# Performance work log

Measured on AMD Instinct MI355X. Metric: run time of the kernel, lower is better.

Reference implementation:

```python
import jax, jax.numpy as jnp
import numpy as np


def setup_inputs() -> dict:
    key = jax.random.key(0)
    ks = jax.random.split(key, 9)
    B, Q, K, F, C = 16, 2048, 2048, 128, 2
    q = jax.random.normal(ks[0], (B, Q, F), dtype=jnp.float32)
    k = jax.random.normal(ks[1], (B, K, F), dtype=jnp.float32)
    v = jax.random.normal(ks[2], (B, K, F), dtype=jnp.float32)
    coords_q = jax.random.uniform(ks[3], (B, Q, C), dtype=jnp.float32)
    coords_k = jax.random.uniform(ks[4], (B, K, C), dtype=jnp.float32)
    attn_mask = jax.random.randint(ks[5], (B, Q, K), 0, 2).astype(jnp.bool_)
    alibi_mask = jax.random.randint(ks[6], (B, Q, K), 0, 2).astype(jnp.bool_)
    bias_scale = jax.random.uniform(ks[7], (1,), dtype=jnp.float32)  # nn.Parameter(torch.rand(1))
    running_mean = jnp.ones((1,), dtype=jnp.float32)  # RunningMeanScaler buffer (eval mode)
    return {"q": q, "k": k, "v": v, "coords_q": coords_q, "coords_k": coords_k,
            "attn_mask": attn_mask, "alibi_mask": alibi_mask,
            "bias_scale": bias_scale, "running_mean": running_mean}


def reference(q, k, v, coords_q, coords_k, attn_mask, alibi_mask, bias_scale, running_mean):
    # [b,q,k] attention logits
    scale = jnp.asarray(k.shape[-1], q.dtype) ** -0.5
    weight_logits = jnp.einsum('bqf,bkf->bqk', q, k) * scale
    # pairwise coordinate distances [b,q,k]
    diff = coords_q[:, :, None, :] - coords_k[:, None, :, :]
    distances = jnp.sqrt(jnp.sum(diff * diff, axis=-1))
    scaled_distances = (distances / running_mean) * bias_scale  # broadcast scalars
    masked_distances = jnp.where(alibi_mask, jnp.zeros((), distances.dtype), scaled_distances)
    weights = jax.nn.softmax(weight_logits, axis=-1)
    masked = jnp.where(attn_mask, jnp.zeros((), weights.dtype), weights - masked_distances)
    attention = jnp.einsum('bqk,bkf->bqf', masked, v)
    return attention
```

## Files before the change

### kernel.cpp

```cpp
#include <hip/hip_runtime.h>
#include <stdint.h>

#define B_  16
#define QL  2048
#define KL  2048
#define FD  128
#define BQ  64
#define BK  32
#define NSTEP (KL/BK)

#define KSTR  136
#define VTOFF 4352
#define VTSTR 36
#define BUFS  8960
#define WS_HALF (B_*KL*FD)

typedef __attribute__((ext_vector_type(8))) short bf16x8;
typedef __attribute__((ext_vector_type(4))) float f32x4;
typedef __attribute__((ext_vector_type(4))) int   i32x4;
typedef __attribute__((ext_vector_type(4))) unsigned int u32x4;

__device__ __forceinline__ unsigned short f2b(float f) {
  union { float f; unsigned u; } x; x.f = f;
  return (unsigned short)((x.u + 0x8000u) >> 16);
}

__device__ __forceinline__ unsigned cvt_pk_bf16(float lo, float hi) {
  unsigned r;
  asm("v_cvt_pk_bf16_f32 %0, %1, %2" : "=v"(r) : "v"(lo), "v"(hi));
  return r;
}

__global__ __launch_bounds__(256) void conv_k(const float* __restrict__ kp,
                                              unsigned short* __restrict__ kb) {
  int idx = (blockIdx.x * 256 + threadIdx.x) * 4;
  float4 u = *(const float4*)(kp + idx);
  ushort4 s4; s4.x = f2b(u.x); s4.y = f2b(u.y); s4.z = f2b(u.z); s4.w = f2b(u.w);
  *(ushort4*)(kb + idx) = s4;
}

__global__ __launch_bounds__(256) void conv_vt(const float* __restrict__ vp,
                                               unsigned short* __restrict__ vt) {
  __shared__ float tl[32 * 132];
  const int t = threadIdx.x, b = blockIdx.x >> 6, kt = blockIdx.x & 63;
  const int r = t >> 3, f0 = (t & 7) * 16;
  const float* src = vp + ((long long)(b * KL + kt * 32 + r)) * FD + f0;
  #pragma unroll
  for (int i = 0; i < 4; ++i)
    *(float4*)&tl[r * 132 + f0 + 4 * i] = *(const float4*)(src + 4 * i);
  __syncthreads();
  const int f = t >> 1, half = t & 1;
  bf16x8 o0, o1;
  #pragma unroll
  for (int j = 0; j < 8; ++j)  o0[j] = (short)f2b(tl[(half * 16 + j) * 132 + f]);
  #pragma unroll
  for (int j = 0; j < 8; ++j)  o1[j] = (short)f2b(tl[(half * 16 + 8 + j) * 132 + f]);
  unsigned short* dst = vt + ((long long)((b * 64 + kt) * FD + f)) * 32 + half * 16;
  *(bf16x8*)dst = o0;
  *(bf16x8*)(dst + 8) = o1;
}

__global__ __launch_bounds__(256, 2) void alibi_attn(
    const unsigned short* __restrict__ kbp,
    const unsigned short* __restrict__ vtp,
    const float* __restrict__ qp,
    const float* __restrict__ cqp,
    const float* __restrict__ ckp,
    const int* __restrict__ amp,
    const int* __restrict__ almp,
    const float* __restrict__ bsp,
    const float* __restrict__ rmp,
    float* __restrict__ outp)
{
  __shared__ unsigned short kv[2 * BUFS];

  const int t    = threadIdx.x;
  const int w    = t >> 6;
  const int lane = t & 63;
  const int l15  = lane & 15;
  const int q4   = lane >> 4;

  const int bid  = blockIdx.x;
  const int xcd  = bid & 7, slot = bid >> 3;
  const int b    = (xcd << 1) | (slot >> 5);
  const int qbase = (slot & 31) * BQ;

  const float bscale = bsp[0] / rmp[0];
  const float sl2 = 0.08838834764831845f * 1.44269504089f;

  const int kr_st = t >> 3, kc_st = (t & 7) * 16;
  const int vf_st = t >> 1, vh_st = (t & 1) * 16;

  {
    const float* qg = qp + ((long long)(b * QL + qbase)) * FD;
    #pragma unroll
    for (int i = 0; i < 8; ++i) {
      int idx = t + 256 * i;
      float4 u = ((const float4*)qg)[idx];
      int row = idx >> 5, col = (idx & 31) * 4;
      ushort4 s4; s4.x = f2b(u.x); s4.y = f2b(u.y); s4.z = f2b(u.z); s4.w = f2b(u.w);
      *(ushort4*)&kv[row * KSTR + col] = s4;
    }
  }
  __syncthreads();
  bf16x8 qfrag[4];
  {
    const int m = w * 16 + l15;
    #pragma unroll
    for (int fs = 0; fs < 4; ++fs)
      qfrag[fs] = *(const bf16x8*)&kv[m * KSTR + fs * 32 + q4 * 8];
  }
  const int qrow = qbase + w * 16 + l15;
  float cqx, cqy;
  {
    float2 c2 = *(const float2*)(cqp + ((long long)(b * QL + qrow)) * 2);
    cqx = c2.x; cqy = c2.y;
  }
  const long long mrow = (long long)(b * QL + qrow) * KL;
  __syncthreads();

  const unsigned short* kgb = kbp + (long long)b * KL * FD;
  const unsigned short* vgb = vtp + (long long)b * KL * FD;

  i32x4 amv[2][2], alv[2][2];
  f32x4 ckf[2][2][2];
  bf16x8 kreg[2][2], vreg[2][2];
  const int klane0 = 4 * q4;
  #pragma unroll
  for (int s = 0; s < 2; ++s) {
    const int k0 = s * 16 + klane0;
    amv[0][s] = __builtin_nontemporal_load((const i32x4*)(amp + mrow + k0));
    alv[0][s] = __builtin_nontemporal_load((const i32x4*)(almp + mrow + k0));
    ckf[0][s][0] = *(const f32x4*)(ckp + ((long long)(b * KL + k0)) * 2);
    ckf[0][s][1] = *(const f32x4*)(ckp + ((long long)(b * KL + k0)) * 2 + 4);
  }
  {
    bf16x8 k0l = *(const bf16x8*)(kgb + kr_st * FD + kc_st);
    bf16x8 k1l = *(const bf16x8*)(kgb + kr_st * FD + kc_st + 8);
    bf16x8 v0l = *(const bf16x8*)(vgb + t * 16);
    bf16x8 v1l = *(const bf16x8*)(vgb + t * 16 + 8);
    *(bf16x8*)&kv[kr_st * KSTR + kc_st]     = k0l;
    *(bf16x8*)&kv[kr_st * KSTR + kc_st + 8] = k1l;
    *(bf16x8*)&kv[VTOFF + vf_st * VTSTR + vh_st]     = v0l;
    *(bf16x8*)&kv[VTOFF + vf_st * VTSTR + vh_st + 8] = v1l;
    kreg[1][0] = *(const bf16x8*)(kgb + (BK + kr_st) * FD + kc_st);
    kreg[1][1] = *(const bf16x8*)(kgb + (BK + kr_st) * FD + kc_st + 8);
    vreg[1][0] = *(const bf16x8*)(vgb + BK * FD + t * 16);
    vreg[1][1] = *(const bf16x8*)(vgb + BK * FD + t * 16 + 8);
  }
  __syncthreads();

  f32x4 O1[8], O2[8];
  #pragma unroll
  for (int n = 0; n < 8; ++n) {
    O1[n] = (f32x4){0.f, 0.f, 0.f, 0.f};
    O2[n] = (f32x4){0.f, 0.f, 0.f, 0.f};
  }
  float lsum = 0.f;

  const int srcA = l15 + ((q4 & 1) << 5);
  const int srcB = srcA + 16;
  const bool lowhalf = (q4 < 2);

  #pragma unroll 2
  for (int kt = 0; kt < NSTEP; ++kt) {
    const int cur = kt & 1, nxt = cur ^ 1;
    const unsigned short* kb = kv + cur * BUFS;
    unsigned short*       nb = kv + nxt * BUFS;

    const int ktf = (kt + 2 < NSTEP) ? (kt + 2) : (NSTEP - 1);
    kreg[cur][0] = *(const bf16x8*)(kgb + (ktf * BK + kr_st) * FD + kc_st);
    kreg[cur][1] = *(const bf16x8*)(kgb + (ktf * BK + kr_st) * FD + kc_st + 8);
    vreg[cur][0] = *(const bf16x8*)(vgb + ktf * (BK * FD) + t * 16);
    vreg[cur][1] = *(const bf16x8*)(vgb + ktf * (BK * FD) + t * 16 + 8);

    const int ktm = (kt + 1 < NSTEP) ? (kt + 1) : kt;
    #pragma unroll
    for (int s = 0; s < 2; ++s) {
      const int kg = ktm * BK + s * 16 + klane0;
      amv[nxt][s] = __builtin_nontemporal_load((const i32x4*)(amp + mrow + kg));
      alv[nxt][s] = __builtin_nontemporal_load((const i32x4*)(almp + mrow + kg));
      ckf[nxt][s][0] = *(const f32x4*)(ckp + ((long long)(b * KL + kg)) * 2);
      ckf[nxt][s][1] = *(const f32x4*)(ckp + ((long long)(b * KL + kg)) * 2 + 4);
    }

    f32x4 S0 = (f32x4){0.f, 0.f, 0.f, 0.f};
    f32x4 S1 = (f32x4){0.f, 0.f, 0.f, 0.f};
    #pragma unroll
    for (int fs = 0; fs < 4; ++fs) {
      bf16x8 kb0 = *(const bf16x8*)&kb[(l15)      * KSTR + fs * 32 + q4 * 8];
      bf16x8 kb1 = *(const bf16x8*)&kb[(16 + l15) * KSTR + fs * 32 + q4 * 8];
      S0 = __builtin_amdgcn_mfma_f32_16x16x32_bf16(kb0, qfrag[fs], S0, 0, 0, 0);
      S1 = __builtin_amdgcn_mfma_f32_16x16x32_bf16(kb1, qfrag[fs], S1, 0, 0, 0);
    }

    float wvv[2][4], tvv[2][4];
    #pragma unroll
    for (int s = 0; s < 2; ++s) {
      const f32x4 Sv = s ? S1 : S0;
      #pragma unroll
      for (int r = 0; r < 4; ++r) {
        float e = __builtin_amdgcn_exp2f(Sv[r] * sl2);
        lsum += e;
        const float ckx = ckf[cur][s][r >> 1][(r & 1) * 2];
        const float cky = ckf[cur][s][r >> 1][(r & 1) * 2 + 1];
        float dx = cqx - ckx, dy = cqy - cky;
        float d  = sqrtf(fmaf(dx, dx, dy * dy)) * bscale;
        int am = amv[cur][s][r], al = alv[cur][s][r];
        wvv[s][r] = am ? 0.f : e;
        tvv[s][r] = (am | al) ? 0.f : d;
      }
    }

    unsigned aX0 = cvt_pk_bf16(wvv[0][0], wvv[0][1]);
    unsigned aX1 = cvt_pk_bf16(wvv[0][2], wvv[0][3]);
    unsigned aX2 = cvt_pk_bf16(wvv[1][0], wvv[1][1]);
    unsigned aX3 = cvt_pk_bf16(wvv[1][2], wvv[1][3]);
    unsigned tX0 = cvt_pk_bf16(tvv[0][0], tvv[0][1]);
    unsigned tX1 = cvt_pk_bf16(tvv[0][2], tvv[0][3]);
    unsigned tX2 = cvt_pk_bf16(tvv[1][0], tvv[1][1]);
    unsigned tX3 = cvt_pk_bf16(tvv[1][2], tvv[1][3]);

    u32x4 wa, ta;
    {
      int y0, y2;
      y0 = __shfl((int)aX0, srcA); y2 = __shfl((int)aX2, srcA);
      wa[0] = (unsigned)(lowhalf ? y0 : y2);
      y0 = __shfl((int)aX1, srcA); y2 = __shfl((int)aX3, srcA);
      wa[1] = (unsigned)(lowhalf ? y0 : y2);
      y0 = __shfl((int)aX0, srcB); y2 = __shfl((int)aX2, srcB);
      wa[2] = (unsigned)(lowhalf ? y0 : y2);
      y0 = __shfl((int)aX1, srcB); y2 = __shfl((int)aX3, srcB);
      wa[3] = (unsigned)(lowhalf ? y0 : y2);
      y0 = __shfl((int)tX0, srcA); y2 = __shfl((int)tX2, srcA);
      ta[0] = (unsigned)(lowhalf ? y0 : y2);
      y0 = __shfl((int)tX1, srcA); y2 = __shfl((int)tX3, srcA);
      ta[1] = (unsigned)(lowhalf ? y0 : y2);
      y0 = __shfl((int)tX0, srcB); y2 = __shfl((int)tX2, srcB);
      ta[2] = (unsigned)(lowhalf ? y0 : y2);
      y0 = __shfl((int)tX1, srcB); y2 = __shfl((int)tX3, srcB);
      ta[3] = (unsigned)(lowhalf ? y0 : y2);
    }
    bf16x8 aw = __builtin_bit_cast(bf16x8, wa);
    bf16x8 at = __builtin_bit_cast(bf16x8, ta);

    #pragma unroll
    for (int n = 0; n < 8; ++n) {
      bf16x8 vb = *(const bf16x8*)&kb[VTOFF + (n * 16 + l15) * VTSTR + q4 * 8];
      O1[n] = __builtin_amdgcn_mfma_f32_16x16x32_bf16(aw, vb, O1[n], 0, 0, 0);
      O2[n] = __builtin_amdgcn_mfma_f32_16x16x32_bf16(at, vb, O2[n], 0, 0, 0);
    }

    *(bf16x8*)&nb[kr_st * KSTR + kc_st]     = kreg[nxt][0];
    *(bf16x8*)&nb[kr_st * KSTR + kc_st + 8] = kreg[nxt][1];
    *(bf16x8*)&nb[VTOFF + vf_st * VTSTR + vh_st]     = vreg[nxt][0];
    *(bf16x8*)&nb[VTOFF + vf_st * VTSTR + vh_st + 8] = vreg[nxt][1];

    asm volatile("s_waitcnt lgkmcnt(0)\n\ts_barrier" ::: "memory");
  }

  lsum += __shfl_xor(lsum, 16, 64);
  lsum += __shfl_xor(lsum, 32, 64);
  float linv[4];
  #pragma unroll
  for (int r = 0; r < 4; ++r) linv[r] = 1.0f / __shfl(lsum, q4 * 4 + r, 64);

  #pragma unroll
  for (int n = 0; n < 8; ++n) {
    #pragma unroll
    for (int r = 0; r < 4; ++r) {
      const int qg_ = qbase + w * 16 + q4 * 4 + r;
      const int f   = n * 16 + l15;
      float val = O1[n][r] * linv[r] - O2[n][r];
      __builtin_nontemporal_store(val, outp + ((long long)(b * QL + qg_)) * FD + f);
    }
  }
}

extern "C" void kernel_launch(void* const* d_in, const int* in_sizes, int n_in,
                              void* d_out, int out_size, void* d_ws, size_t ws_size,
                              hipStream_t stream) {
  const float* q   = (const float*)d_in[0];
  const float* k   = (const float*)d_in[1];
  const float* v   = (const float*)d_in[2];
  const float* cq  = (const float*)d_in[3];
  const float* ck  = (const float*)d_in[4];
  const int*   am  = (const int*)d_in[5];
  const int*   alm = (const int*)d_in[6];
  const float* bs  = (const float*)d_in[7];
  const float* rm  = (const float*)d_in[8];
  float*       out = (float*)d_out;

  unsigned short* kb = (unsigned short*)d_ws;
  unsigned short* vt = kb + WS_HALF;

  hipLaunchKernelGGL(conv_k,  dim3(WS_HALF / 1024), dim3(256), 0, stream, k, kb);
  hipLaunchKernelGGL(conv_vt, dim3(B_ * 64),        dim3(256), 0, stream, v, vt);

  dim3 grid(B_ * (QL / BQ));
  dim3 block(256);
  hipLaunchKernelGGL(alibi_attn, grid, block, 0, stream,
                     kb, vt, q, cq, ck, am, alm, bs, rm, out);
}
```

Before: 676.0 us.

## Split key dimension across two blocks and combine partial sums in extra kernel

Splits the key loop into two halves handled by separate blocks (split-K), doubling the grid from 512 to 1024 blocks. Each block writes its unnormalized partial O1/O2 and row sums to workspace, and a new combine kernel sums them and normalizes. Launch bounds rise to 4 waves per SIMD to allow more resident blocks. This is meant to fix low occupancy and poor CU utilization, at the cost of extra global traffic for the partials and an extra launch. It falls back to the old path if the workspace is too small.

```diff
diff --git a/kernel.cpp b/kernel.cpp
--- a/kernel.cpp
+++ b/kernel.cpp
@@ -60,7 +60,8 @@
   *(bf16x8*)(dst + 8) = o1;
 }
 
-__global__ __launch_bounds__(256, 2) void alibi_attn(
+template<int SPLIT>
+__global__ __launch_bounds__(256, 4) void alibi_attn(
     const unsigned short* __restrict__ kbp,
     const unsigned short* __restrict__ vtp,
     const float* __restrict__ qp,
@@ -70,9 +71,14 @@
     const int* __restrict__ almp,
     const float* __restrict__ bsp,
     const float* __restrict__ rmp,
-    float* __restrict__ outp)
+    float* __restrict__ outp,
+    float* __restrict__ o1p,
+    float* __restrict__ o2p,
+    float* __restrict__ lsp)
 {
   __shared__ unsigned short kv[2 * BUFS];
+
+  const int NT = SPLIT ? (NSTEP / 2) : NSTEP;
 
   const int t    = threadIdx.x;
   const int w    = t >> 6;
@@ -81,9 +87,12 @@
   const int q4   = lane >> 4;
 
   const int bid  = blockIdx.x;
-  const int xcd  = bid & 7, slot = bid >> 3;
+  const int half = SPLIT ? (bid >> 9) : 0;
+  const int bid5 = bid & 511;
+  const int xcd  = bid5 & 7, slot = bid5 >> 3;
   const int b    = (xcd << 1) | (slot >> 5);
   const int qbase = (slot & 31) * BQ;
+  const int kt0  = half * NT;
 
   const float bscale = bsp[0] / rmp[0];
   const float sl2 = 0.08838834764831845f * 1.44269504089f;
@@ -128,25 +137,25 @@
   const int klane0 = 4 * q4;
   #pragma unroll
   for (int s = 0; s < 2; ++s) {
-    const int k0 = s * 16 + klane0;
+    const int k0 = kt0 * BK + s * 16 + klane0;
     amv[0][s] = __builtin_nontemporal_load((const i32x4*)(amp + mrow + k0));
     alv[0][s] = __builtin_nontemporal_load((const i32x4*)(almp + mrow + k0));
     ckf[0][s][0] = *(const f32x4*)(ckp + ((long long)(b * KL + k0)) * 2);
     ckf[0][s][1] = *(const f32x4*)(ckp + ((long long)(b * KL + k0)) * 2 + 4);
   }
   {
-    bf16x8 k0l = *(const bf16x8*)(kgb + kr_st * FD + kc_st);
-    bf16x8 k1l = *(const bf16x8*)(kgb + kr_st * FD + kc_st + 8);
-    bf16x8 v0l = *(const bf16x8*)(vgb + t * 16);
-    bf16x8 v1l = *(const bf16x8*)(vgb + t * 16 + 8);
+    bf16x8 k0l = *(const bf16x8*)(kgb + (kt0 * BK + kr_st) * FD + kc_st);
+    bf16x8 k1l = *(const bf16x8*)(kgb + (kt0 * BK + kr_st) * FD + kc_st + 8);
+    bf16x8 v0l = *(const bf16x8*)(vgb + kt0 * (BK * FD) + t * 16);
+    bf16x8 v1l = *(const bf16x8*)(vgb + kt0 * (BK * FD) + t * 16 + 8);
     *(bf16x8*)&kv[kr_st * KSTR + kc_st]     = k0l;
     *(bf16x8*)&kv[kr_st * KSTR + kc_st + 8] = k1l;
     *(bf16x8*)&kv[VTOFF + vf_st * VTSTR + vh_st]     = v0l;
     *(bf16x8*)&kv[VTOFF + vf_st * VTSTR + vh_st + 8] = v1l;
-    kreg[1][0] = *(const bf16x8*)(kgb + (BK + kr_st) * FD + kc_st);
-    kreg[1][1] = *(const bf16x8*)(kgb + (BK + kr_st) * FD + kc_st + 8);
-    vreg[1][0] = *(const bf16x8*)(vgb + BK * FD + t * 16);
-    vreg[1][1] = *(const bf16x8*)(vgb + BK * FD + t * 16 + 8);
+    kreg[1][0] = *(const bf16x8*)(kgb + ((kt0 + 1) * BK + kr_st) * FD + kc_st);
+    kreg[1][1] = *(const bf16x8*)(kgb + ((kt0 + 1) * BK + kr_st) * FD + kc_st + 8);
+    vreg[1][0] = *(const bf16x8*)(vgb + (kt0 + 1) * (BK * FD) + t * 16);
+    vreg[1][1] = *(const bf16x8*)(vgb + (kt0 + 1) * (BK * FD) + t * 16 + 8);
   }
   __syncthreads();
 
@@ -163,18 +172,18 @@
   const bool lowhalf = (q4 < 2);
 
   #pragma unroll 2
-  for (int kt = 0; kt < NSTEP; ++kt) {
+  for (int kt = 0; kt < NT; ++kt) {
     const int cur = kt & 1, nxt = cur ^ 1;
     const unsigned short* kb = kv + cur * BUFS;
     unsigned short*       nb = kv + nxt * BUFS;
 
-    const int ktf = (kt + 2 < NSTEP) ? (kt + 2) : (NSTEP - 1);
+    const int ktf = kt0 + ((kt + 2 < NT) ? (kt + 2) : (NT - 1));
     kreg[cur][0] = *(const bf16x8*)(kgb + (ktf * BK + kr_st) * FD + kc_st);
     kreg[cur][1] = *(const bf16x8*)(kgb + (ktf * BK + kr_st) * FD + kc_st + 8);
     vreg[cur][0] = *(const bf16x8*)(vgb + ktf * (BK * FD) + t * 16);
     vreg[cur][1] = *(const bf16x8*)(vgb + ktf * (BK * FD) + t * 16 + 8);
 
-    const int ktm = (kt + 1 < NSTEP) ? (kt + 1) : kt;
+    const int ktm = kt0 + ((kt + 1 < NT) ? (kt + 1) : (NT - 1));
     #pragma unroll
     for (int s = 0; s < 2; ++s) {
       const int kg = ktm * BK + s * 16 + klane0;
@@ -261,20 +270,55 @@
 
   lsum += __shfl_xor(lsum, 16, 64);
   lsum += __shfl_xor(lsum, 32, 64);
-  float linv[4];
-  #pragma unroll
-  for (int r = 0; r < 4; ++r) linv[r] = 1.0f / __shfl(lsum, q4 * 4 + r, 64);
-
-  #pragma unroll
-  for (int n = 0; n < 8; ++n) {
-    #pragma unroll
-    for (int r = 0; r < 4; ++r) {
-      const int qg_ = qbase + w * 16 + q4 * 4 + r;
-      const int f   = n * 16 + l15;
-      float val = O1[n][r] * linv[r] - O2[n][r];
-      __builtin_nontemporal_store(val, outp + ((long long)(b * QL + qg_)) * FD + f);
-    }
-  }
+
+  if (SPLIT) {
+    if (q4 == 0) lsp[(half * B_ + b) * QL + qrow] = lsum;
+    #pragma unroll
+    for (int n = 0; n < 8; ++n) {
+      #pragma unroll
+      for (int r = 0; r < 4; ++r) {
+        const int qg_ = qbase + w * 16 + q4 * 4 + r;
+        const long long idx =
+            ((long long)((half * B_ + b) * QL + qg_)) * FD + n * 16 + l15;
+        __builtin_nontemporal_store(O1[n][r], o1p + idx);
+        __builtin_nontemporal_store(O2[n][r], o2p + idx);
+      }
+    }
+  } else {
+    float linv[4];
+    #pragma unroll
+    for (int r = 0; r < 4; ++r) linv[r] = 1.0f / __shfl(lsum, q4 * 4 + r, 64);
+    #pragma unroll
+    for (int n = 0; n < 8; ++n) {
+      #pragma unroll
+      for (int r = 0; r < 4; ++r) {
+        const int qg_ = qbase + w * 16 + q4 * 4 + r;
+        const int f   = n * 16 + l15;
+        float val = O1[n][r] * linv[r] - O2[n][r];
+        __builtin_nontemporal_store(val, outp + ((long long)(b * QL + qg_)) * FD + f);
+      }
+    }
+  }
+}
+
+#define HALFE (B_*QL*FD/4)
+__global__ __launch_bounds__(256) void combine(const float* __restrict__ o1p,
+                                               const float* __restrict__ o2p,
+                                               const float* __restrict__ lsp,
+                                               float* __restrict__ outp) {
+  const int e = blockIdx.x * 256 + threadIdx.x;
+  const int row = e >> 5;
+  const float li = 1.0f / (lsp[row] + lsp[B_ * QL + row]);
+  f32x4 a0 = __builtin_nontemporal_load((const f32x4*)o1p + e);
+  f32x4 a1 = __builtin_nontemporal_load((const f32x4*)o1p + HALFE + e);
+  f32x4 b0 = __builtin_nontemporal_load((const f32x4*)o2p + e);
+  f32x4 b1 = __builtin_nontemporal_load((const f32x4*)o2p + HALFE + e);
+  f32x4 o;
+  o[0] = (a0[0] + a1[0]) * li - (b0[0] + b1[0]);
+  o[1] = (a0[1] + a1[1]) * li - (b0[1] + b1[1]);
+  o[2] = (a0[2] + a1[2]) * li - (b0[2] + b1[2]);
+  o[3] = (a0[3] + a1[3]) * li - (b0[3] + b1[3]);
+  __builtin_nontemporal_store(o, (f32x4*)outp + e);
 }
 
 extern "C" void kernel_launch(void* const* d_in, const int* in_sizes, int n_in,
@@ -297,8 +341,21 @@
   hipLaunchKernelGGL(conv_k,  dim3(WS_HALF / 1024), dim3(256), 0, stream, k, kb);
   hipLaunchKernelGGL(conv_vt, dim3(B_ * 64),        dim3(256), 0, stream, v, vt);
 
-  dim3 grid(B_ * (QL / BQ));
-  dim3 block(256);
-  hipLaunchKernelGGL(alibi_attn, grid, block, 0, stream,
-                     kb, vt, q, cq, ck, am, alm, bs, rm, out);
-}
+  const size_t conv_bytes = (size_t)2 * WS_HALF * sizeof(unsigned short);
+  const size_t oele = (size_t)2 * B_ * QL * FD;
+  const size_t need = conv_bytes + 2 * oele * sizeof(float)
+                    + (size_t)2 * B_ * QL * sizeof(float);
+  float* o1p = (float*)((char*)d_ws + conv_bytes);
+  float* o2p = o1p + oele;
+  float* lsp = o2p + oele;
+
+  if (ws_size >= need) {
+    hipLaunchKernelGGL((alibi_attn<1>), dim3(2 * B_ * (QL / BQ)), dim3(256), 0, stream,
+                       kb, vt, q, cq, ck, am, alm, bs, rm, out, o1p, o2p, lsp);
+    hipLaunchKernelGGL(combine, dim3(B_ * QL * FD / 4 / 256), dim3(256), 0, stream,
+                       o1p, o2p, lsp, out);
+  } else {
+    hipLaunchKernelGGL((alibi_attn<0>), dim3(B_ * (QL / BQ)), dim3(256), 0, stream,
+                       kb, vt, q, cq, ck, am, alm, bs, rm, out, o1p, o2p, lsp);
+  }
+}
```

New measurement: 1.072 ms. +58.6%, slower.

## Pre-pack attention and alibi masks into bitmasks in a separate kernel

Applied to the files above, without the earlier changes.

Adds a pack_masks kernel that turns the int32 attn and alibi masks into per-row bitmasks: one bit for attn and one for attn-or-alibi, grouped in 32-key words. The attention kernel then loads one 8-byte word per 32-key step instead of four 16-byte int vectors per lane, and tests bits. The masks are still read in full once by the packing kernel, so total global traffic does not drop. The gain would come from taking the nontemporal mask loads out of the MFMA inner loop, in exchange for an extra launch and a workspace write and read.

```diff
diff --git a/kernel.cpp b/kernel.cpp
--- a/kernel.cpp
+++ b/kernel.cpp
@@ -14,11 +14,14 @@
 #define VTSTR 36
 #define BUFS  8960
 #define WS_HALF (B_*KL*FD)
+#define NROW  (B_*QL)
+#define WPR   (KL/32)
 
 typedef __attribute__((ext_vector_type(8))) short bf16x8;
 typedef __attribute__((ext_vector_type(4))) float f32x4;
 typedef __attribute__((ext_vector_type(4))) int   i32x4;
 typedef __attribute__((ext_vector_type(4))) unsigned int u32x4;
+typedef __attribute__((ext_vector_type(2))) unsigned int u32x2;
 
 __device__ __forceinline__ unsigned short f2b(float f) {
   union { float f; unsigned u; } x; x.f = f;
@@ -60,14 +63,35 @@
   *(bf16x8*)(dst + 8) = o1;
 }
 
+__global__ __launch_bounds__(256) void pack_masks(const int* __restrict__ amp,
+                                                  const int* __restrict__ almp,
+                                                  u32x2* __restrict__ out) {
+  const int row  = blockIdx.x * 4 + (threadIdx.x >> 6);
+  const int lane = threadIdx.x & 63;
+  const long long base = (long long)row * KL;
+  u32x2* orow = out + (long long)row * WPR;
+  #pragma unroll 4
+  for (int j = 0; j < 32; ++j) {
+    int a = __builtin_nontemporal_load(amp  + base + j * 64 + lane);
+    int l = __builtin_nontemporal_load(almp + base + j * 64 + lane);
+    unsigned long long ab = __ballot(a != 0);
+    unsigned long long ob = ab | __ballot(l != 0);
+    if (lane == 0) {
+      u32x4 pk;
+      pk[0] = (unsigned)ab;         pk[1] = (unsigned)ob;
+      pk[2] = (unsigned)(ab >> 32); pk[3] = (unsigned)(ob >> 32);
+      *(u32x4*)&orow[2 * j] = pk;
+    }
+  }
+}
+
 __global__ __launch_bounds__(256, 2) void alibi_attn(
     const unsigned short* __restrict__ kbp,
     const unsigned short* __restrict__ vtp,
+    const u32x2* __restrict__ pmp,
     const float* __restrict__ qp,
     const float* __restrict__ cqp,
     const float* __restrict__ ckp,
-    const int* __restrict__ amp,
-    const int* __restrict__ almp,
     const float* __restrict__ bsp,
     const float* __restrict__ rmp,
     float* __restrict__ outp)
@@ -116,21 +140,20 @@
     float2 c2 = *(const float2*)(cqp + ((long long)(b * QL + qrow)) * 2);
     cqx = c2.x; cqy = c2.y;
   }
-  const long long mrow = (long long)(b * QL + qrow) * KL;
+  const long long mwrow = (long long)(b * QL + qrow) * WPR;
   __syncthreads();
 
   const unsigned short* kgb = kbp + (long long)b * KL * FD;
   const unsigned short* vgb = vtp + (long long)b * KL * FD;
 
-  i32x4 amv[2][2], alv[2][2];
+  u32x2 mw[2];
   f32x4 ckf[2][2][2];
   bf16x8 kreg[2][2], vreg[2][2];
   const int klane0 = 4 * q4;
+  mw[0] = pmp[mwrow];
   #pragma unroll
   for (int s = 0; s < 2; ++s) {
     const int k0 = s * 16 + klane0;
-    amv[0][s] = __builtin_nontemporal_load((const i32x4*)(amp + mrow + k0));
-    alv[0][s] = __builtin_nontemporal_load((const i32x4*)(almp + mrow + k0));
     ckf[0][s][0] = *(const f32x4*)(ckp + ((long long)(b * KL + k0)) * 2);
     ckf[0][s][1] = *(const f32x4*)(ckp + ((long long)(b * KL + k0)) * 2 + 4);
   }
@@ -175,11 +198,10 @@
     vreg[cur][1] = *(const bf16x8*)(vgb + ktf * (BK * FD) + t * 16 + 8);
 
     const int ktm = (kt + 1 < NSTEP) ? (kt + 1) : kt;
+    mw[nxt] = pmp[mwrow + ktm];
     #pragma unroll
     for (int s = 0; s < 2; ++s) {
       const int kg = ktm * BK + s * 16 + klane0;
-      amv[nxt][s] = __builtin_nontemporal_load((const i32x4*)(amp + mrow + kg));
-      alv[nxt][s] = __builtin_nontemporal_load((const i32x4*)(almp + mrow + kg));
       ckf[nxt][s][0] = *(const f32x4*)(ckp + ((long long)(b * KL + kg)) * 2);
       ckf[nxt][s][1] = *(const f32x4*)(ckp + ((long long)(b * KL + kg)) * 2 + 4);
     }
@@ -194,6 +216,7 @@
       S1 = __builtin_amdgcn_mfma_f32_16x16x32_bf16(kb1, qfrag[fs], S1, 0, 0, 0);
     }
 
+    const unsigned ab = mw[cur][0], ob = mw[cur][1];
     float wvv[2][4], tvv[2][4];
     #pragma unroll
     for (int s = 0; s < 2; ++s) {
@@ -206,9 +229,9 @@
         const float cky = ckf[cur][s][r >> 1][(r & 1) * 2 + 1];
         float dx = cqx - ckx, dy = cqy - cky;
         float d  = sqrtf(fmaf(dx, dx, dy * dy)) * bscale;
-        int am = amv[cur][s][r], al = alv[cur][s][r];
-        wvv[s][r] = am ? 0.f : e;
-        tvv[s][r] = (am | al) ? 0.f : d;
+        const int bit = s * 16 + klane0 + r;
+        wvv[s][r] = ((ab >> bit) & 1u) ? 0.f : e;
+        tvv[s][r] = ((ob >> bit) & 1u) ? 0.f : d;
       }
     }
 
@@ -293,12 +316,14 @@
 
   unsigned short* kb = (unsigned short*)d_ws;
   unsigned short* vt = kb + WS_HALF;
-
-  hipLaunchKernelGGL(conv_k,  dim3(WS_HALF / 1024), dim3(256), 0, stream, k, kb);
-  hipLaunchKernelGGL(conv_vt, dim3(B_ * 64),        dim3(256), 0, stream, v, vt);
+  u32x2*          pm = (u32x2*)(vt + WS_HALF);
+
+  hipLaunchKernelGGL(conv_k,     dim3(WS_HALF / 1024), dim3(256), 0, stream, k, kb);
+  hipLaunchKernelGGL(conv_vt,    dim3(B_ * 64),        dim3(256), 0, stream, v, vt);
+  hipLaunchKernelGGL(pack_masks, dim3(NROW / 4),       dim3(256), 0, stream, am, alm, pm);
 
   dim3 grid(B_ * (QL / BQ));
   dim3 block(256);
   hipLaunchKernelGGL(alibi_attn, grid, block, 0, stream,
-                     kb, vt, q, cq, ck, am, alm, bs, rm, out);
-}
+                     kb, vt, pm, q, cq, ck, bs, rm, out);
+}
```

Result: slower. 754.4 us (+11.6%).

## Process K tiles in pairs with precomputed mask bitmasks and distance fragments

Applied to the files above, without the earlier changes.

Restructures the main loop to handle two 32-key tiles per iteration, doubling the LDS ring to four buffers so there is one barrier per pair. Mask and distance work for the next pair is done a pair ahead: attention and alibi masks are compressed into 32-bit bitmasks shared across the wave, and the distance bf16 fragments are built and shuffled ahead of use. This takes mask and distance latency off the critical path and halves barrier count. The costs are higher LDS use (about 70KB per block, which may limit two blocks per CU), more register pressure, and extra cross-lane shuffles per tile.

```diff
diff --git a/kernel.cpp b/kernel.cpp
--- a/kernel.cpp
+++ b/kernel.cpp
@@ -8,6 +8,7 @@
 #define BQ  64
 #define BK  32
 #define NSTEP (KL/BK)
+#define NPAIR (NSTEP/2)
 
 #define KSTR  136
 #define VTOFF 4352
@@ -58,6 +59,57 @@
   unsigned short* dst = vt + ((long long)((b * 64 + kt) * FD + f)) * 32 + half * 16;
   *(bf16x8*)dst = o0;
   *(bf16x8*)(dst + 8) = o1;
+}
+
+__device__ __forceinline__ void digest_tile(
+    const i32x4* ram, const i32x4* ral, const f32x4 (*rck)[2],
+    float cqx, float cqy, float bscale, int klane0,
+    int srcA, int srcB, bool lowhalf,
+    unsigned& amw_o, u32x4& ta_o)
+{
+  unsigned pb = 0, ob = 0;
+  #pragma unroll
+  for (int s = 0; s < 2; ++s)
+    #pragma unroll
+    for (int r = 0; r < 4; ++r) {
+      const unsigned bm = 1u << (s * 16 + klane0 + r);
+      pb |= ram[s][r] ? bm : 0u;
+      ob |= (ram[s][r] | ral[s][r]) ? bm : 0u;
+    }
+  pb |= (unsigned)__shfl_xor((int)pb, 16, 64);
+  pb |= (unsigned)__shfl_xor((int)pb, 32, 64);
+  ob |= (unsigned)__shfl_xor((int)ob, 16, 64);
+  ob |= (unsigned)__shfl_xor((int)ob, 32, 64);
+
+  float tvv[2][4];
+  #pragma unroll
+  for (int s = 0; s < 2; ++s)
+    #pragma unroll
+    for (int r = 0; r < 4; ++r) {
+      const float ckx = rck[s][r >> 1][(r & 1) * 2];
+      const float cky = rck[s][r >> 1][(r & 1) * 2 + 1];
+      float dx = cqx - ckx, dy = cqy - cky;
+      float d  = sqrtf(fmaf(dx, dx, dy * dy)) * bscale;
+      tvv[s][r] = ((ob >> (s * 16 + klane0 + r)) & 1u) ? 0.f : d;
+    }
+  unsigned tX0 = cvt_pk_bf16(tvv[0][0], tvv[0][1]);
+  unsigned tX1 = cvt_pk_bf16(tvv[0][2], tvv[0][3]);
+  unsigned tX2 = cvt_pk_bf16(tvv[1][0], tvv[1][1]);
+  unsigned tX3 = cvt_pk_bf16(tvv[1][2], tvv[1][3]);
+  u32x4 ta;
+  {
+    int y0, y2;
+    y0 = __shfl((int)tX0, srcA, 64); y2 = __shfl((int)tX2, srcA, 64);
+    ta[0] = (unsigned)(lowhalf ? y0 : y2);
+    y0 = __shfl((int)tX1, srcA, 64); y2 = __shfl((int)tX3, srcA, 64);
+    ta[1] = (unsigned)(lowhalf ? y0 : y2);
+    y0 = __shfl((int)tX0, srcB, 64); y2 = __shfl((int)tX2, srcB, 64);
+    ta[2] = (unsigned)(lowhalf ? y0 : y2);
+    y0 = __shfl((int)tX1, srcB, 64); y2 = __shfl((int)tX3, srcB, 64);
+    ta[3] = (unsigned)(lowhalf ? y0 : y2);
+  }
+  amw_o = pb;
+  ta_o  = ta;
 }
 
 __global__ __launch_bounds__(256, 2) void alibi_attn(
@@ -72,7 +124,7 @@
     const float* __restrict__ rmp,
     float* __restrict__ outp)
 {
-  __shared__ unsigned short kv[2 * BUFS];
+  __shared__ unsigned short kv[4 * BUFS];
 
   const int t    = threadIdx.x;
   const int w    = t >> 6;
@@ -90,6 +142,31 @@
 
   const int kr_st = t >> 3, kc_st = (t & 7) * 16;
   const int vf_st = t >> 1, vh_st = (t & 1) * 16;
+  const int klane0 = 4 * q4;
+
+  const int qrow = qbase + w * 16 + l15;
+  const long long mrow = (long long)(b * QL + qrow) * KL;
+
+  const unsigned short* kgb = kbp + (long long)b * KL * FD;
+  const unsigned short* vgb = vtp + (long long)b * KL * FD;
+
+  float cqx, cqy;
+  {
+    float2 c2 = *(const float2*)(cqp + ((long long)(b * QL + qrow)) * 2);
+    cqx = c2.x; cqy = c2.y;
+  }
+  i32x4 ram[2][2], ral[2][2];
+  f32x4 rck[2][2][2];
+  #pragma unroll
+  for (int tt = 0; tt < 2; ++tt)
+    #pragma unroll
+    for (int s = 0; s < 2; ++s) {
+      const int kg = tt * BK + s * 16 + klane0;
+      ram[tt][s] = __builtin_nontemporal_load((const i32x4*)(amp + mrow + kg));
+      ral[tt][s] = __builtin_nontemporal_load((const i32x4*)(almp + mrow + kg));
+      rck[tt][s][0] = *(const f32x4*)(ckp + ((long long)(b * KL + kg)) * 2);
+      rck[tt][s][1] = *(const f32x4*)(ckp + ((long long)(b * KL + kg)) * 2 + 4);
+    }
 
   {
     const float* qg = qp + ((long long)(b * QL + qbase)) * FD;
@@ -110,43 +187,27 @@
     for (int fs = 0; fs < 4; ++fs)
       qfrag[fs] = *(const bf16x8*)&kv[m * KSTR + fs * 32 + q4 * 8];
   }
-  const int qrow = qbase + w * 16 + l15;
-  float cqx, cqy;
-  {
-    float2 c2 = *(const float2*)(cqp + ((long long)(b * QL + qrow)) * 2);
-    cqx = c2.x; cqy = c2.y;
-  }
-  const long long mrow = (long long)(b * QL + qrow) * KL;
   __syncthreads();
 
-  const unsigned short* kgb = kbp + (long long)b * KL * FD;
-  const unsigned short* vgb = vtp + (long long)b * KL * FD;
-
-  i32x4 amv[2][2], alv[2][2];
-  f32x4 ckf[2][2][2];
-  bf16x8 kreg[2][2], vreg[2][2];
-  const int klane0 = 4 * q4;
-  #pragma unroll
-  for (int s = 0; s < 2; ++s) {
-    const int k0 = s * 16 + klane0;
-    amv[0][s] = __builtin_nontemporal_load((const i32x4*)(amp + mrow + k0));
-    alv[0][s] = __builtin_nontemporal_load((const i32x4*)(almp + mrow + k0));
-    ckf[0][s][0] = *(const f32x4*)(ckp + ((long long)(b * KL + k0)) * 2);
-    ckf[0][s][1] = *(const f32x4*)(ckp + ((long long)(b * KL + k0)) * 2 + 4);
-  }
-  {
-    bf16x8 k0l = *(const bf16x8*)(kgb + kr_st * FD + kc_st);
-    bf16x8 k1l = *(const bf16x8*)(kgb + kr_st * FD + kc_st + 8);
-    bf16x8 v0l = *(const bf16x8*)(vgb + t * 16);
-    bf16x8 v1l = *(const bf16x8*)(vgb + t * 16 + 8);
-    *(bf16x8*)&kv[kr_st * KSTR + kc_st]     = k0l;
-    *(bf16x8*)&kv[kr_st * KSTR + kc_st + 8] = k1l;
-    *(bf16x8*)&kv[VTOFF + vf_st * VTSTR + vh_st]     = v0l;
-    *(bf16x8*)&kv[VTOFF + vf_st * VTSTR + vh_st + 8] = v1l;
-    kreg[1][0] = *(const bf16x8*)(kgb + (BK + kr_st) * FD + kc_st);
-    kreg[1][1] = *(const bf16x8*)(kgb + (BK + kr_st) * FD + kc_st + 8);
-    vreg[1][0] = *(const bf16x8*)(vgb + BK * FD + t * 16);
-    vreg[1][1] = *(const bf16x8*)(vgb + BK * FD + t * 16 + 8);
+  const int srcA = l15 + ((q4 & 1) << 5);
+  const int srcB = srcA + 16;
+  const bool lowhalf = (q4 < 2);
+
+  unsigned dg_amw[2][2];
+  u32x4    dg_ta[2][2];
+  #pragma unroll
+  for (int tt = 0; tt < 2; ++tt) {
+    bf16x8 k0l = *(const bf16x8*)(kgb + (tt * BK + kr_st) * FD + kc_st);
+    bf16x8 k1l = *(const bf16x8*)(kgb + (tt * BK + kr_st) * FD + kc_st + 8);
+    bf16x8 v0l = *(const bf16x8*)(vgb + tt * (BK * FD) + t * 16);
+    bf16x8 v1l = *(const bf16x8*)(vgb + tt * (BK * FD) + t * 16 + 8);
+    unsigned short* wbuf = kv + tt * BUFS;
+    *(bf16x8*)&wbuf[kr_st * KSTR + kc_st]     = k0l;
+    *(bf16x8*)&wbuf[kr_st * KSTR + kc_st + 8] = k1l;
+    *(bf16x8*)&wbuf[VTOFF + vf_st * VTSTR + vh_st]     = v0l;
+    *(bf16x8*)&wbuf[VTOFF + vf_st * VTSTR + vh_st + 8] = v1l;
+    digest_tile(ram[tt], ral[tt], rck[tt], cqx, cqy, bscale, klane0,
+                srcA, srcB, lowhalf, dg_amw[0][tt], dg_ta[0][tt]);
   }
   __syncthreads();
 
@@ -158,103 +219,95 @@
   }
   float lsum = 0.f;
 
-  const int srcA = l15 + ((q4 & 1) << 5);
-  const int srcB = srcA + 16;
-  const bool lowhalf = (q4 < 2);
-
   #pragma unroll 2
-  for (int kt = 0; kt < NSTEP; ++kt) {
-    const int cur = kt & 1, nxt = cur ^ 1;
-    const unsigned short* kb = kv + cur * BUFS;
-    unsigned short*       nb = kv + nxt * BUFS;
-
-    const int ktf = (kt + 2 < NSTEP) ? (kt + 2) : (NSTEP - 1);
-    kreg[cur][0] = *(const bf16x8*)(kgb + (ktf * BK + kr_st) * FD + kc_st);
-    kreg[cur][1] = *(const bf16x8*)(kgb + (ktf * BK + kr_st) * FD + kc_st + 8);
-    vreg[cur][0] = *(const bf16x8*)(vgb + ktf * (BK * FD) + t * 16);
-    vreg[cur][1] = *(const bf16x8*)(vgb + ktf * (BK * FD) + t * 16 + 8);
-
-    const int ktm = (kt + 1 < NSTEP) ? (kt + 1) : kt;
-    #pragma unroll
-    for (int s = 0; s < 2; ++s) {
-      const int kg = ktm * BK + s * 16 + klane0;
-      amv[nxt][s] = __builtin_nontemporal_load((const i32x4*)(amp + mrow + kg));
-      alv[nxt][s] = __builtin_nontemporal_load((const i32x4*)(almp + mrow + kg));
-      ckf[nxt][s][0] = *(const f32x4*)(ckp + ((long long)(b * KL + kg)) * 2);
-      ckf[nxt][s][1] = *(const f32x4*)(ckp + ((long long)(b * KL + kg)) * 2 + 4);
-    }
-
-    f32x4 S0 = (f32x4){0.f, 0.f, 0.f, 0.f};
-    f32x4 S1 = (f32x4){0.f, 0.f, 0.f, 0.f};
-    #pragma unroll
-    for (int fs = 0; fs < 4; ++fs) {
-      bf16x8 kb0 = *(const bf16x8*)&kb[(l15)      * KSTR + fs * 32 + q4 * 8];
-      bf16x8 kb1 = *(const bf16x8*)&kb[(16 + l15) * KSTR + fs * 32 + q4 * 8];
-      S0 = __builtin_amdgcn_mfma_f32_16x16x32_bf16(kb0, qfrag[fs], S0, 0, 0, 0);
-      S1 = __builtin_amdgcn_mfma_f32_16x16x32_bf16(kb1, qfrag[fs], S1, 0, 0, 0);
-    }
-
-    float wvv[2][4], tvv[2][4];
-    #pragma unroll
-    for (int s = 0; s < 2; ++s) {
-      const f32x4 Sv = s ? S1 : S0;
+  for (int i = 0; i < NPAIR; ++i) {
+    const int cur = i & 1, nxt = cur ^ 1;
+    const unsigned short* rb = kv + (cur ? 2 * BUFS : 0);
+    unsigned short*       wb = kv + (nxt ? 2 * BUFS : 0);
+    const int tp = (i + 1 < NPAIR) ? (i + 1) : (NPAIR - 1);
+
+    bf16x8 krg[2][2], vrg[2][2];
+    #pragma unroll
+    for (int tt = 0; tt < 2; ++tt) {
+      const int tg = 2 * tp + tt;
+      krg[tt][0] = *(const bf16x8*)(kgb + (tg * BK + kr_st) * FD + kc_st);
+      krg[tt][1] = *(const bf16x8*)(kgb + (tg * BK + kr_st) * FD + kc_st + 8);
+      vrg[tt][0] = *(const bf16x8*)(vgb + tg * (BK * FD) + t * 16);
+      vrg[tt][1] = *(const bf16x8*)(vgb + tg * (BK * FD) + t * 16 + 8);
       #pragma unroll
-      for (int r = 0; r < 4; ++r) {
-        float e = __builtin_amdgcn_exp2f(Sv[r] * sl2);
-        lsum += e;
-        const float ckx = ckf[cur][s][r >> 1][(r & 1) * 2];
-        const float cky = ckf[cur][s][r >> 1][(r & 1) * 2 + 1];
-        float dx = cqx - ckx, dy = cqy - cky;
-        float d  = sqrtf(fmaf(dx, dx, dy * dy)) * bscale;
-        int am = amv[cur][s][r], al = alv[cur][s][r];
-        wvv[s][r] = am ? 0.f : e;
-        tvv[s][r] = (am | al) ? 0.f : d;
-      }
-    }
-
-    unsigned aX0 = cvt_pk_bf16(wvv[0][0], wvv[0][1]);
-    unsigned aX1 = cvt_pk_bf16(wvv[0][2], wvv[0][3]);
-    unsigned aX2 = cvt_pk_bf16(wvv[1][0], wvv[1][1]);
-    unsigned aX3 = cvt_pk_bf16(wvv[1][2], wvv[1][3]);
-    unsigned tX0 = cvt_pk_bf16(tvv[0][0], tvv[0][1]);
-    unsigned tX1 = cvt_pk_bf16(tvv[0][2], tvv[0][3]);
-    unsigned tX2 = cvt_pk_bf16(tvv[1][0], tvv[1][1]);
-    unsigned tX3 = cvt_pk_bf16(tvv[1][2], tvv[1][3]);
-
-    u32x4 wa, ta;
-    {
-      int y0, y2;
-      y0 = __shfl((int)aX0, srcA); y2 = __shfl((int)aX2, srcA);
-      wa[0] = (unsigned)(lowhalf ? y0 : y2);
-      y0 = __shfl((int)aX1, srcA); y2 = __shfl((int)aX3, srcA);
-      wa[1] = (unsigned)(lowhalf ? y0 : y2);
-      y0 = __shfl((int)aX0, srcB); y2 = __shfl((int)aX2, srcB);
-      wa[2] = (unsigned)(lowhalf ? y0 : y2);
-      y0 = __shfl((int)aX1, srcB); y2 = __shfl((int)aX3, srcB);
-      wa[3] = (unsigned)(lowhalf ? y0 : y2);
-      y0 = __shfl((int)tX0, srcA); y2 = __shfl((int)tX2, srcA);
-      ta[0] = (unsigned)(lowhalf ? y0 : y2);
-      y0 = __shfl((int)tX1, srcA); y2 = __shfl((int)tX3, srcA);
-      ta[1] = (unsigned)(lowhalf ? y0 : y2);
-      y0 = __shfl((int)tX0, srcB); y2 = __shfl((int)tX2, srcB);
-      ta[2] = (unsigned)(lowhalf ? y0 : y2);
-      y0 = __shfl((int)tX1, srcB); y2 = __shfl((int)tX3, srcB);
-      ta[3] = (unsigned)(lowhalf ? y0 : y2);
-    }
-    bf16x8 aw = __builtin_bit_cast(bf16x8, wa);
-    bf16x8 at = __builtin_bit_cast(bf16x8, ta);
-
-    #pragma unroll
-    for (int n = 0; n < 8; ++n) {
-      bf16x8 vb = *(const bf16x8*)&kb[VTOFF + (n * 16 + l15) * VTSTR + q4 * 8];
-      O1[n] = __builtin_amdgcn_mfma_f32_16x16x32_bf16(aw, vb, O1[n], 0, 0, 0);
-      O2[n] = __builtin_amdgcn_mfma_f32_16x16x32_bf16(at, vb, O2[n], 0, 0, 0);
-    }
-
-    *(bf16x8*)&nb[kr_st * KSTR + kc_st]     = kreg[nxt][0];
-    *(bf16x8*)&nb[kr_st * KSTR + kc_st + 8] = kreg[nxt][1];
-    *(bf16x8*)&nb[VTOFF + vf_st * VTSTR + vh_st]     = vreg[nxt][0];
-    *(bf16x8*)&nb[VTOFF + vf_st * VTSTR + vh_st + 8] = vreg[nxt][1];
+      for (int s = 0; s < 2; ++s) {
+        const int kg = tg * BK + s * 16 + klane0;
+        ram[tt][s] = __builtin_nontemporal_load((const i32x4*)(amp + mrow + kg));
+        ral[tt][s] = __builtin_nontemporal_load((const i32x4*)(almp + mrow + kg));
+        rck[tt][s][0] = *(const f32x4*)(ckp + ((long long)(b * KL + kg)) * 2);
+        rck[tt][s][1] = *(const f32x4*)(ckp + ((long long)(b * KL + kg)) * 2 + 4);
+      }
+    }
+
+    #pragma unroll
+    for (int tt = 0; tt < 2; ++tt) {
+      const unsigned short* buf = rb + tt * BUFS;
+
+      f32x4 S0 = (f32x4){0.f, 0.f, 0.f, 0.f};
+      f32x4 S1 = (f32x4){0.f, 0.f, 0.f, 0.f};
+      #pragma unroll
+      for (int fs = 0; fs < 4; ++fs) {
+        bf16x8 kb0 = *(const bf16x8*)&buf[(l15)      * KSTR + fs * 32 + q4 * 8];
+        bf16x8 kb1 = *(const bf16x8*)&buf[(16 + l15) * KSTR + fs * 32 + q4 * 8];
+        S0 = __builtin_amdgcn_mfma_f32_16x16x32_bf16(kb0, qfrag[fs], S0, 0, 0, 0);
+        S1 = __builtin_amdgcn_mfma_f32_16x16x32_bf16(kb1, qfrag[fs], S1, 0, 0, 0);
+      }
+
+      const unsigned amw = dg_amw[cur][tt];
+      float wvv[2][4];
+      #pragma unroll
+      for (int s = 0; s < 2; ++s) {
+        const f32x4 Sv = s ? S1 : S0;
+        #pragma unroll
+        for (int r = 0; r < 4; ++r) {
+          float e = __builtin_amdgcn_exp2f(Sv[r] * sl2);
+          lsum += e;
+          wvv[s][r] = ((amw >> (s * 16 + klane0 + r)) & 1u) ? 0.f : e;
+        }
+      }
+      unsigned aX0 = cvt_pk_bf16(wvv[0][0], wvv[0][1]);
+      unsigned aX1 = cvt_pk_bf16(wvv[0][2], wvv[0][3]);
+      unsigned aX2 = cvt_pk_bf16(wvv[1][0], wvv[1][1]);
+      unsigned aX3 = cvt_pk_bf16(wvv[1][2], wvv[1][3]);
+      u32x4 wa;
+      {
+        int y0, y2;
+        y0 = __shfl((int)aX0, srcA, 64); y2 = __shfl((int)aX2, srcA, 64);
+        wa[0] = (unsigned)(lowhalf ? y0 : y2);
+        y0 = __shfl((int)aX1, srcA, 64); y2 = __shfl((int)aX3, srcA, 64);
+        wa[1] = (unsigned)(lowhalf ? y0 : y2);
+        y0 = __shfl((int)aX0, srcB, 64); y2 = __shfl((int)aX2, srcB, 64);
+        wa[2] = (unsigned)(lowhalf ? y0 : y2);
+        y0 = __shfl((int)aX1, srcB, 64); y2 = __shfl((int)aX3, srcB, 64);
+        wa[3] = (unsigned)(lowhalf ? y0 : y2);
+      }
+      bf16x8 aw = __builtin_bit_cast(bf16x8, wa);
+      bf16x8 at = __builtin_bit_cast(bf16x8, dg_ta[cur][tt]);
+
+      #pragma unroll
+      for (int n = 0; n < 8; ++n) {
+        bf16x8 vb = *(const bf16x8*)&buf[VTOFF + (n * 16 + l15) * VTSTR + q4 * 8];
+        O1[n] = __builtin_amdgcn_mfma_f32_16x16x32_bf16(aw, vb, O1[n], 0, 0, 0);
+        O2[n] = __builtin_amdgcn_mfma_f32_16x16x32_bf16(at, vb, O2[n], 0, 0, 0);
+      }
+
+      digest_tile(ram[tt], ral[tt], rck[tt], cqx, cqy, bscale, klane0,
+                  srcA, srcB, lowhalf, dg_amw[nxt][tt], dg_ta[nxt][tt]);
+    }
+
+    #pragma unroll
+    for (int tt = 0; tt < 2; ++tt) {
+      unsigned short* wbuf = wb + tt * BUFS;
+      *(bf16x8*)&wbuf[kr_st * KSTR + kc_st]     = krg[tt][0];
+      *(bf16x8*)&wbuf[kr_st * KSTR + kc_st + 8] = krg[tt][1];
+      *(bf16x8*)&wbuf[VTOFF + vf_st * VTSTR + vh_st]     = vrg[tt][0];
+      *(bf16x8*)&wbuf[VTOFF + vf_st * VTSTR + vh_st + 8] = vrg[tt][1];
+    }
 
     asm volatile("s_waitcnt lgkmcnt(0)\n\ts_barrier" ::: "memory");
   }
```

Result: slower. 709.4 us (+4.9%).
